# Performance work log

Measured on AMD Instinct MI355X. Metric: run time of the kernel, lower is better.

Reference implementation:

```python
import jax, jax.numpy as jnp
import numpy as np

B, NSEQ, SEQ_PER = 2, 4, 256
S = NSEQ * SEQ_PER            # total sequence (stocks interleaved along seq dim)
D, H, HD = 1024, 16, 64       # d_model, nhead, head_dim
HD2, HD4 = HD // 2, HD // 4
DFF = 4096
LAMBDA_INIT = 0.2             # lambda_init_fn(0) = 0.8 - 0.6*exp(0)
SCALING = 1.0 / float(np.sqrt(HD2))
EPS_DEF = float(np.finfo(np.float32).eps)   # torch RMSNorm default eps (eps=None)
EPS_ATTN = 1e-5


def _rms(x, w, eps):
    return x * jax.lax.rsqrt(jnp.mean(x * x, axis=-1, keepdims=True) + eps) * w


def _rope(x, fc):
    # x: (B, T, NSEQ, 2H, HD2); fc: (T, HD4, 2) holding (cos, sin)
    xr = x.reshape(x.shape[:-1] + (HD4, 2))
    c = fc[None, :, None, None, :, 0]
    s = fc[None, :, None, None, :, 1]
    x0, x1 = xr[..., 0], xr[..., 1]
    return jnp.stack([x0 * c - x1 * s, x0 * s + x1 * c], axis=-1).reshape(x.shape)


def setup_inputs():
    key = jax.random.key(0)
    ks = jax.random.split(key, 16)
    def w(i, shape, std=0.02):
        return jax.random.normal(ks[i], shape, jnp.float32) * std
    # true RoPE table for seq_per_stock-1 positions
    t = jnp.arange(SEQ_PER - 1, dtype=jnp.float32)[:, None]
    inv = 1.0 / (10000.0 ** (jnp.arange(HD4, dtype=jnp.float32) / HD4))
    ang = t * inv[None, :]
    return {
        "x": jax.random.normal(ks[0], (B, S, D), jnp.float32),
        "freqs_cis": jnp.stack([jnp.cos(ang), jnp.sin(ang)], axis=-1),
        "w_norm1": jnp.ones((D,), jnp.float32),
        "w_norm2": jnp.ones((D,), jnp.float32),
        "Wq": w(1, (H * HD, D)), "bq": jnp.zeros((H * HD,), jnp.float32),
        "Wk": w(2, (H * HD, D)), "bk": jnp.zeros((H * HD,), jnp.float32),
        "Wv": w(3, (H * HD, D)), "bv": jnp.zeros((H * HD,), jnp.float32),
        "Wo": w(4, (D, H * HD)), "bo": jnp.zeros((D,), jnp.float32),
        "lq1": w(5, (HD2,), 0.1), "lk1": w(6, (HD2,), 0.1),
        "lq2": w(7, (HD2,), 0.1), "lk2": w(8, (HD2,), 0.1),
        "w_attn_norm": jnp.ones((HD,), jnp.float32),
        "Wg": w(9, (2 * DFF, D)), "bg": jnp.zeros((2 * DFF,), jnp.float32),
        "Wout": w(10, (D, DFF)), "bout": jnp.zeros((D,), jnp.float32),
    }


def reference(x, freqs_cis, w_norm1, w_norm2, Wq, bq, Wk, bk, Wv, bv, Wo, bo,
              lq1, lk1, lq2, lk2, w_attn_norm, Wg, bg, Wout, bout):
    Bz, Sz, _ = x.shape
    h = _rms(x, w_norm1, EPS_DEF)
    q = (h @ Wq.T + bq).reshape(Bz, SEQ_PER, NSEQ, 2 * H, HD2)
    k = (h @ Wk.T + bk).reshape(Bz, SEQ_PER, NSEQ, 2 * H, HD2)
    v = (h @ Wv.T + bv).reshape(Bz, Sz, H, HD).transpose(0, 2, 1, 3)   # (B,H,S,HD), interleaved order
    # RoPE on all but the first per-stock timestep; same freqs for every stock
    q = jnp.concatenate([q[:, :1], _rope(q[:, 1:], freqs_cis)], axis=1)
    k = jnp.concatenate([k[:, :1], _rope(k[:, 1:], freqs_cis)], axis=1)
    # reorder q/k to stock-major flat sequence (torch permute(0,4,1,2,3)+reshape)
    q = q.transpose(0, 2, 1, 3, 4).reshape(Bz, Sz, 2 * H, HD2).transpose(0, 2, 1, 3)
    k = k.transpose(0, 2, 1, 3, 4).reshape(Bz, Sz, 2 * H, HD2).transpose(0, 2, 1, 3)
    scores = jnp.einsum('bhqd,bhkd->bhqk', q, k) * SCALING              # (B,2H,S,S)
    causal = jnp.triu(jnp.ones((SEQ_PER, SEQ_PER), bool), 1)
    mask = jnp.tile(causal, (NSEQ, NSEQ))   # block-tiled causal, as torch .repeat
    att = jnp.sign(scores) * jax.nn.softmax(
        jnp.where(mask, -1e30, jnp.abs(scores)), axis=-1)
    lam = jnp.exp(jnp.sum(lk1 * lq1)) - jnp.exp(jnp.sum(lk2 * lq2)) + LAMBDA_INIT
    att = att.reshape(Bz, H, 2, Sz, Sz)
    a1, a2 = att[:, :, 0], att[:, :, 1]
    G = jnp.mean(a1, axis=-2, keepdims=True)          # mean over queries, broadcast back
    a = jnp.where(mask, 0.0, a1 - lam * a2 + lam * G)
    ao = jnp.einsum('bhqk,bhkd->bhqd', a, v)          # v kept in interleaved order (faithful to source)
    ao = _rms(ao, w_attn_norm, EPS_ATTN)
    ao = ao.reshape(Bz, Sz, H * HD)  # flat reinterpret (B,H,S,HD)->(B,S,H*HD), matches torch reshape chain
    x = x + ao @ Wo.T + bo
    h2 = _rms(x, w_norm2, EPS_DEF)
    u, vg = jnp.split(h2 @ Wg.T + bg, 2, axis=-1)
    return x + (u * jax.nn.silu(vg)) @ Wout.T + bout
```

## Files before the change

kernel.cpp:

```cpp
#include <hip/hip_runtime.h>

#define LAMBDA_INIT 0.2f
#define SCALING 0.17677669529663687f
#define EPS_DEF 1.1920928955078125e-07f
#define EPS_ATTN 1e-5f

typedef unsigned short us4 __attribute__((ext_vector_type(4)));
typedef unsigned short us8v __attribute__((ext_vector_type(8)));
typedef float f32x4 __attribute__((ext_vector_type(4)));
typedef float f32x2 __attribute__((ext_vector_type(2)));
typedef __bf16 bf16x8 __attribute__((ext_vector_type(8)));

#define MFMA16(a, b, c) __builtin_amdgcn_mfma_f32_16x16x32_bf16((a), (b), (c), 0, 0, 0)

__device__ __forceinline__ float bf2f(unsigned short u) {
    unsigned int x = ((unsigned int)u) << 16;
    return __builtin_bit_cast(float, x);
}
__device__ __forceinline__ unsigned short f2bf(float f) {
    unsigned int x = __builtin_bit_cast(unsigned int, f);
    x += 0x7fffu + ((x >> 16) & 1u);
    return (unsigned short)(x >> 16);
}
__device__ __forceinline__ void split8(f32x4 a, f32x4 b, us8v& hi, us8v& lo) {
#pragma unroll
    for (int u = 0; u < 4; u++) {
        unsigned short h = f2bf(a[u]);
        hi[u] = h; lo[u] = f2bf(a[u] - bf2f(h));
        unsigned short h2 = f2bf(b[u]);
        hi[4 + u] = h2; lo[4 + u] = f2bf(b[u] - bf2f(h2));
    }
}
__device__ __forceinline__ bf16x8 ldb(const unsigned short* p) {
    return __builtin_bit_cast(bf16x8, *(const us8v*)p);
}
__device__ __forceinline__ f32x4 rope4(f32x4 v, const float* __restrict__ fc, int p, int dd) {
    if (p == 0) return v;
    int d4 = (dd & 31) >> 1;
    f32x4 f = *(const f32x4*)(fc + ((size_t)(p - 1) * 16 + d4) * 2);
    f32x4 o;
    o[0] = v[0] * f[0] - v[1] * f[1];
    o[1] = v[0] * f[1] + v[1] * f[0];
    o[2] = v[2] * f[2] - v[3] * f[3];
    o[3] = v[2] * f[3] + v[3] * f[2];
    return o;
}

__device__ __forceinline__ float wave_sum(float v) {
#pragma unroll
    for (int o = 32; o > 0; o >>= 1) v += __shfl_down(v, o);
    return v;
}
__device__ __forceinline__ float block_sum(float v, float* red4) {
    int wv = threadIdx.x >> 6;
    float w = wave_sum(v);
    __syncthreads();
    if ((threadIdx.x & 63) == 0) red4[wv] = w;
    __syncthreads();
    return red4[0] + red4[1] + red4[2] + red4[3];
}

__global__ __launch_bounds__(256) void prep(float* __restrict__ G, float* __restrict__ lamp,
                                            const float* lq1, const float* lk1,
                                            const float* lq2, const float* lk2) {
    int i = (blockIdx.x * 256 + threadIdx.x) * 4;
    G[i] = 0.f; G[i + 1] = 0.f; G[i + 2] = 0.f; G[i + 3] = 0.f;
    if (blockIdx.x == 0 && threadIdx.x == 0) {
        float a = 0.f, c = 0.f;
        for (int d = 0; d < 32; d++) {
            a += lq1[d] * lk1[d];
            c += lq2[d] * lk2[d];
        }
        *lamp = expf(a) - expf(c) + LAMBDA_INIT;
    }
}

__global__ __launch_bounds__(256) void cvt_wsplit(
        const float* __restrict__ s0, const float* __restrict__ s1,
        const float* __restrict__ s2, const float* __restrict__ s3,
        unsigned short* __restrict__ h0, unsigned short* __restrict__ l0,
        unsigned short* __restrict__ h1p, unsigned short* __restrict__ l1p,
        unsigned short* __restrict__ h2p, unsigned short* __restrict__ l2p,
        unsigned short* __restrict__ d3, int n4) {
    const int z = blockIdx.y;
    int i = blockIdx.x * 256 + threadIdx.x;
    if (i >= n4) return;
    if (z == 3) {
        f32x4 v = ((const f32x4*)s3)[i];
        us4 o;
#pragma unroll
        for (int u = 0; u < 4; u++) o[u] = f2bf(v[u]);
        ((us4*)d3)[i] = o;
        return;
    }
    const float* s = (z == 0) ? s0 : (z == 1) ? s1 : s2;
    unsigned short* hi = (z == 0) ? h0 : (z == 1) ? h1p : h2p;
    unsigned short* lo = (z == 0) ? l0 : (z == 1) ? l1p : l2p;
    f32x4 v = ((const f32x4*)s)[i];
    us4 h, l;
#pragma unroll
    for (int u = 0; u < 4; u++) {
        h[u] = f2bf(v[u]);
        l[u] = f2bf(v[u] - bf2f(h[u]));
    }
    ((us4*)hi)[i] = h;
    ((us4*)lo)[i] = l;
}

__global__ __launch_bounds__(256) void cvt_gate2(const float* __restrict__ Wg,
                                                 unsigned short* __restrict__ WuB,
                                                 unsigned short* __restrict__ WvB, int n4) {
    const int z = blockIdx.y;
    const float* s = Wg + (size_t)z * 4194304;
    unsigned short* d = z ? WvB : WuB;
    int i = blockIdx.x * 256 + threadIdx.x;
    if (i >= n4) return;
    f32x4 v = ((const f32x4*)s)[i];
    us4 o;
#pragma unroll
    for (int u = 0; u < 4; u++) o[u] = f2bf(v[u]);
    ((us4*)d)[i] = o;
}

__global__ __launch_bounds__(256) void cvt_bf16(const float* __restrict__ s,
                                                unsigned short* __restrict__ d, int n4) {
    int i = blockIdx.x * 256 + threadIdx.x;
    if (i >= n4) return;
    f32x4 v = ((const f32x4*)s)[i];
    us4 o;
#pragma unroll
    for (int u = 0; u < 4; u++) o[u] = f2bf(v[u]);
    ((us4*)d)[i] = o;
}

template <int OUTBF>
__global__ __launch_bounds__(256) void rms_kernel(const float* __restrict__ x,
                                                  const float* __restrict__ w,
                                                  void* __restrict__ out, float eps) {
    int row = blockIdx.x;
    int tid = threadIdx.x;
    size_t base = (size_t)row * 1024 + tid * 4;
    f32x4 v = *(const f32x4*)(x + base);
    float ss = v[0]*v[0] + v[1]*v[1] + v[2]*v[2] + v[3]*v[3];
    __shared__ float red4[4];
    float tot = block_sum(ss, red4);
    float r = rsqrtf(tot * (1.0f / 1024.f) + eps);
    f32x4 wv = *(const f32x4*)(w + tid * 4);
    if (OUTBF) {
        us4 o;
#pragma unroll
        for (int i = 0; i < 4; i++) o[i] = f2bf(v[i] * r * wv[i]);
        *(us4*)((unsigned short*)out + base) = o;
    } else {
        f32x4 o;
#pragma unroll
        for (int i = 0; i < 4; i++) o[i] = v[i] * r * wv[i];
        *(f32x4*)((float*)out + base) = o;
    }
}

__global__ __launch_bounds__(256) void rms_split(const float* __restrict__ x,
                                                 const float* __restrict__ w,
                                                 unsigned short* __restrict__ hh,
                                                 unsigned short* __restrict__ hl, float eps) {
    int row = blockIdx.x;
    int tid = threadIdx.x;
    size_t base = (size_t)row * 1024 + tid * 4;
    f32x4 v = *(const f32x4*)(x + base);
    float ss = v[0]*v[0] + v[1]*v[1] + v[2]*v[2] + v[3]*v[3];
    __shared__ float red4[4];
    float tot = block_sum(ss, red4);
    float r = rsqrtf(tot * (1.0f / 1024.f) + eps);
    f32x4 wv = *(const f32x4*)(w + tid * 4);
    us4 oh, ol;
#pragma unroll
    for (int i = 0; i < 4; i++) {
        float val = v[i] * r * wv[i];
        oh[i] = f2bf(val);
        ol[i] = f2bf(val - bf2f(oh[i]));
    }
    *(us4*)(hh + base) = oh;
    *(us4*)(hl + base) = ol;
}

__global__ __launch_bounds__(256) void gemm_qkv_ps(
        const unsigned short* __restrict__ AH, const unsigned short* __restrict__ AL,
        const unsigned short* __restrict__ WqH, const unsigned short* __restrict__ WqL,
        const unsigned short* __restrict__ WkH, const unsigned short* __restrict__ WkL,
        const unsigned short* __restrict__ WvH, const unsigned short* __restrict__ WvL,
        const float* __restrict__ bq, const float* __restrict__ bk, const float* __restrict__ bv,
        float* __restrict__ Yq, float* __restrict__ Yk, float* __restrict__ Yv) {
    const int z = blockIdx.z;
    const unsigned short* BH = (z == 0) ? WqH : (z == 1) ? WkH : WvH;
    const unsigned short* BL = (z == 0) ? WqL : (z == 1) ? WkL : WvL;
    const float* bias = (z == 0) ? bq : (z == 1) ? bk : bv;
    float* out        = (z == 0) ? Yq : (z == 1) ? Yk : Yv;
    const int K = 1024, N = 1024;
    __shared__ __align__(16) unsigned short Ah[64][72];
    __shared__ __align__(16) unsigned short Al[64][72];
    __shared__ __align__(16) unsigned short Bh[64][72];
    __shared__ __align__(16) unsigned short Bl[64][72];
    const int t = threadIdx.x;
    const int bm = blockIdx.x, bn = blockIdx.y;
    const int lane = t & 63, w = t >> 6;
    const int wr = w >> 1, wc = w & 1;
    const int l15 = lane & 15, lg = lane >> 4;
    const int sr = t >> 2, sc = (t & 3) * 16;

    const unsigned short* AgH = AH + (size_t)(bm * 64 + sr) * K + sc;
    const unsigned short* AgL = AL + (size_t)(bm * 64 + sr) * K + sc;
    const unsigned short* BgH = BH + (size_t)(bn * 64 + sr) * K + sc;
    const unsigned short* BgL = BL + (size_t)(bn * 64 + sr) * K + sc;

    f32x4 acc[2][2] = {};

    us8v ah0 = *(const us8v*)AgH, ah1 = *(const us8v*)(AgH + 8);
    us8v al0 = *(const us8v*)AgL, al1 = *(const us8v*)(AgL + 8);
    us8v bh0 = *(const us8v*)BgH, bh1 = *(const us8v*)(BgH + 8);
    us8v bl0 = *(const us8v*)BgL, bl1 = *(const us8v*)(BgL + 8);

    for (int k0 = 0; k0 < K; k0 += 64) {
        __syncthreads();
        *(us8v*)&Ah[sr][sc] = ah0; *(us8v*)&Ah[sr][sc + 8] = ah1;
        *(us8v*)&Al[sr][sc] = al0; *(us8v*)&Al[sr][sc + 8] = al1;
        *(us8v*)&Bh[sr][sc] = bh0; *(us8v*)&Bh[sr][sc + 8] = bh1;
        *(us8v*)&Bl[sr][sc] = bl0; *(us8v*)&Bl[sr][sc + 8] = bl1;
        __syncthreads();
        if (k0 + 64 < K) {
            const int kn = k0 + 64;
            ah0 = *(const us8v*)(AgH + kn); ah1 = *(const us8v*)(AgH + kn + 8);
            al0 = *(const us8v*)(AgL + kn); al1 = *(const us8v*)(AgL + kn + 8);
            bh0 = *(const us8v*)(BgH + kn); bh1 = *(const us8v*)(BgH + kn + 8);
            bl0 = *(const us8v*)(BgL + kn); bl1 = *(const us8v*)(BgL + kn + 8);
        }
#pragma unroll
        for (int kk = 0; kk < 2; kk++) {
            bf16x8 afh[2], afl[2], bfh[2], bfl[2];
#pragma unroll
            for (int mi = 0; mi < 2; mi++) {
                afh[mi] = ldb(&Ah[wr * 32 + mi * 16 + l15][kk * 32 + lg * 8]);
                afl[mi] = ldb(&Al[wr * 32 + mi * 16 + l15][kk * 32 + lg * 8]);
            }
#pragma unroll
            for (int ni = 0; ni < 2; ni++) {
                bfh[ni] = ldb(&Bh[wc * 32 + ni * 16 + l15][kk * 32 + lg * 8]);
                bfl[ni] = ldb(&Bl[wc * 32 + ni * 16 + l15][kk * 32 + lg * 8]);
            }
#pragma unroll
            for (int mi = 0; mi < 2; mi++)
#pragma unroll
                for (int ni = 0; ni < 2; ni++) {
                    acc[mi][ni] = MFMA16(afl[mi], bfh[ni], acc[mi][ni]);
                    acc[mi][ni] = MFMA16(afh[mi], bfl[ni], acc[mi][ni]);
                    acc[mi][ni] = MFMA16(afh[mi], bfh[ni], acc[mi][ni]);
                }
        }
    }

    const int rbase = bm * 64 + wr * 32 + (lg << 2);
    const int cbase = bn * 64 + wc * 32 + l15;
#pragma unroll
    for (int mi = 0; mi < 2; mi++) {
#pragma unroll
        for (int ni = 0; ni < 2; ni++) {
            int col = cbase + ni * 16;
            float bb = bias[col];
#pragma unroll
            for (int r = 0; r < 4; r++) {
                int row = rbase + mi * 16 + r;
                out[(size_t)row * N + col] = acc[mi][ni][r] + bb;
            }
        }
    }
}

__global__ __launch_bounds__(256) void gemm_mfma_wb(const unsigned short* __restrict__ A,
                                                    const unsigned short* __restrict__ Bt,
                                                    const float* __restrict__ bias,
                                                    const float* __restrict__ res,
                                                    float* __restrict__ out,
                                                    int M, int N, int K) {
    __shared__ __align__(16) unsigned short As[64][136];
    __shared__ __align__(16) unsigned short Bs[64][136];
    const int t = threadIdx.x;
    const int bm = blockIdx.x, bn = blockIdx.y;
    const int lane = t & 63, w = t >> 6;
    const int wr = w >> 1, wc = w & 1;
    const int l15 = lane & 15, lg = lane >> 4;
    const int sr = t >> 2, sc = (t & 3) * 32;

    const unsigned short* Ag = A + (size_t)(bm * 64 + sr) * K + sc;
    const unsigned short* Bg = Bt + (size_t)(bn * 64 + sr) * K + sc;

    f32x4 acc[2][2] = {};

    us8v a0 = *(const us8v*)Ag,        a1 = *(const us8v*)(Ag + 8);
    us8v a2 = *(const us8v*)(Ag + 16), a3 = *(const us8v*)(Ag + 24);
    us8v b0 = *(const us8v*)Bg,        b1 = *(const us8v*)(Bg + 8);
    us8v b2 = *(const us8v*)(Bg + 16), b3 = *(const us8v*)(Bg + 24);

    for (int k0 = 0; k0 < K; k0 += 128) {
        __syncthreads();
        *(us8v*)&As[sr][sc]      = a0;
        *(us8v*)&As[sr][sc + 8]  = a1;
        *(us8v*)&As[sr][sc + 16] = a2;
        *(us8v*)&As[sr][sc + 24] = a3;
        *(us8v*)&Bs[sr][sc]      = b0;
        *(us8v*)&Bs[sr][sc + 8]  = b1;
        *(us8v*)&Bs[sr][sc + 16] = b2;
        *(us8v*)&Bs[sr][sc + 24] = b3;
        __syncthreads();
        if (k0 + 128 < K) {
            const int kn = k0 + 128;
            a0 = *(const us8v*)(Ag + kn);      a1 = *(const us8v*)(Ag + kn + 8);
            a2 = *(const us8v*)(Ag + kn + 16); a3 = *(const us8v*)(Ag + kn + 24);
            b0 = *(const us8v*)(Bg + kn);      b1 = *(const us8v*)(Bg + kn + 8);
            b2 = *(const us8v*)(Bg + kn + 16); b3 = *(const us8v*)(Bg + kn + 24);
        }
#pragma unroll
        for (int kk = 0; kk < 4; kk++) {
            bf16x8 af[2], bf[2];
#pragma unroll
            for (int mi = 0; mi < 2; mi++)
                af[mi] = ldb(&As[wr * 32 + mi * 16 + l15][kk * 32 + lg * 8]);
#pragma unroll
            for (int ni = 0; ni < 2; ni++)
                bf[ni] = ldb(&Bs[wc * 32 + ni * 16 + l15][kk * 32 + lg * 8]);
#pragma unroll
            for (int mi = 0; mi < 2; mi++)
#pragma unroll
                for (int ni = 0; ni < 2; ni++)
                    acc[mi][ni] = MFMA16(af[mi], bf[ni], acc[mi][ni]);
        }
    }

    const int rbase = bm * 64 + wr * 32 + (lg << 2);
    const int cbase = bn * 64 + wc * 32 + l15;
#pragma unroll
    for (int mi = 0; mi < 2; mi++) {
#pragma unroll
        for (int ni = 0; ni < 2; ni++) {
            int col = cbase + ni * 16;
            float bb = bias[col];
#pragma unroll
            for (int r = 0; r < 4; r++) {
                int row = rbase + mi * 16 + r;
                size_t oi = (size_t)row * N + col;
                out[oi] = acc[mi][ni][r] + bb + res[oi];
            }
        }
    }
}

__global__ __launch_bounds__(256) void gemm_gate_wb(const unsigned short* __restrict__ A,
                                                    const unsigned short* __restrict__ WuB,
                                                    const unsigned short* __restrict__ WvB,
                                                    const float* __restrict__ bg,
                                                    unsigned short* __restrict__ mlp) {
    __shared__ __align__(16) unsigned short As[128][72];
    __shared__ __align__(16) unsigned short BsU[64][72];
    __shared__ __align__(16) unsigned short BsV[64][72];
    const int t = threadIdx.x;
    const int bm = blockIdx.x, bn = blockIdx.y;
    const int lane = t & 63, w = t >> 6;
    const int wr = w >> 1, wc = w & 1;
    const int l15 = lane & 15, lg = lane >> 4;
    const int sr = t >> 2, sc = (t & 3) * 16;

    const unsigned short* Ag  = A + (size_t)(bm * 128 + sr) * 1024 + sc;
    const unsigned short* Ag2 = Ag + (size_t)64 * 1024;
    const unsigned short* BgU = WuB + (size_t)(bn * 64 + sr) * 1024 + sc;
    const unsigned short* BgV = WvB + (size_t)(bn * 64 + sr) * 1024 + sc;

    f32x4 accU[4][2] = {};
    f32x4 accV[4][2] = {};

    us8v a0 = *(const us8v*)Ag,  a1 = *(const us8v*)(Ag + 8);
    us8v a2 = *(const us8v*)Ag2, a3 = *(const us8v*)(Ag2 + 8);
    us8v u0 = *(const us8v*)BgU, u1 = *(const us8v*)(BgU + 8);
    us8v v0 = *(const us8v*)BgV, v1 = *(const us8v*)(BgV + 8);

    for (int k0 = 0; k0 < 1024; k0 += 64) {
        __syncthreads();
        *(us8v*)&As[sr][sc]          = a0;
        *(us8v*)&As[sr][sc + 8]      = a1;
        *(us8v*)&As[sr + 64][sc]     = a2;
        *(us8v*)&As[sr + 64][sc + 8] = a3;
        *(us8v*)&BsU[sr][sc]         = u0;
        *(us8v*)&BsU[sr][sc + 8]     = u1;
        *(us8v*)&BsV[sr][sc]         = v0;
        *(us8v*)&BsV[sr][sc + 8]     = v1;
        __syncthreads();
        if (k0 + 64 < 1024) {
            const int kn = k0 + 64;
            a0 = *(const us8v*)(Ag + kn);  a1 = *(const us8v*)(Ag + kn + 8);
            a2 = *(const us8v*)(Ag2 + kn); a3 = *(const us8v*)(Ag2 + kn + 8);
            u0 = *(const us8v*)(BgU + kn); u1 = *(const us8v*)(BgU + kn + 8);
            v0 = *(const us8v*)(BgV + kn); v1 = *(const us8v*)(BgV + kn + 8);
        }
#pragma unroll
        for (int kk = 0; kk < 2; kk++) {
            bf16x8 af[4], bu[2], bv2[2];
#pragma unroll
            for (int mi = 0; mi < 4; mi++)
                af[mi] = ldb(&As[wr * 64 + mi * 16 + l15][kk * 32 + lg * 8]);
#pragma unroll
            for (int ni = 0; ni < 2; ni++) {
                bu[ni]  = ldb(&BsU[wc * 32 + ni * 16 + l15][kk * 32 + lg * 8]);
                bv2[ni] = ldb(&BsV[wc * 32 + ni * 16 + l15][kk * 32 + lg * 8]);
            }
#pragma unroll
            for (int mi = 0; mi < 4; mi++)
#pragma unroll
                for (int ni = 0; ni < 2; ni++) {
                    accU[mi][ni] = MFMA16(af[mi], bu[ni], accU[mi][ni]);
                    accV[mi][ni] = MFMA16(af[mi], bv2[ni], accV[mi][ni]);
                }
        }
    }

    const int rbase = bm * 128 + wr * 64 + (lg << 2);
    const int cbase = bn * 64 + wc * 32 + l15;
#pragma unroll
    for (int mi = 0; mi < 4; mi++) {
#pragma unroll
        for (int ni = 0; ni < 2; ni++) {
            int col = cbase + ni * 16;
            float bu_ = bg[col], bv_ = bg[4096 + col];
#pragma unroll
            for (int r = 0; r < 4; r++) {
                int row = rbase + mi * 16 + r;
                float u = accU[mi][ni][r] + bu_;
                float v = accV[mi][ni][r] + bv_;
                float s = v / (1.f + __expf(-v));
                mlp[(size_t)row * 4096 + col] = f2bf(u * s);
            }
        }
    }
}

__global__ __launch_bounds__(256) void rope_split_k(const float* __restrict__ Yk,
                                                    const float* __restrict__ fc,
                                                    unsigned short* __restrict__ KhG,
                                                    unsigned short* __restrict__ KlG) {
    int t = blockIdx.x;
    int s = t & 1023;
    int p = s >> 2;
    int c0 = threadIdx.x * 4;
    const float* y = Yk + (size_t)t * 1024 + c0;
    float v0 = y[0], v1 = y[1], v2 = y[2], v3 = y[3];
    if (p > 0) {
        int d4 = (c0 & 31) >> 1;
        f32x4 f = *(const f32x4*)(fc + ((size_t)(p - 1) * 16 + d4) * 2);
        float w0 = v0 * f[0] - v1 * f[1];
        float w1 = v0 * f[1] + v1 * f[0];
        float w2 = v2 * f[2] - v3 * f[3];
        float w3 = v2 * f[3] + v3 * f[2];
        v0 = w0; v1 = w1; v2 = w2; v3 = w3;
    }
    us4 hi, lo;
    hi[0] = f2bf(v0); lo[0] = f2bf(v0 - bf2f(hi[0]));
    hi[1] = f2bf(v1); lo[1] = f2bf(v1 - bf2f(hi[1]));
    hi[2] = f2bf(v2); lo[2] = f2bf(v2 - bf2f(hi[2]));
    hi[3] = f2bf(v3); lo[3] = f2bf(v3 - bf2f(hi[3]));
    *(us4*)(KhG + (size_t)t * 1024 + c0) = hi;
    *(us4*)(KlG + (size_t)t * 1024 + c0) = lo;
}

__global__ __launch_bounds__(256) void v_split_t(const float* __restrict__ Yv,
                                                 unsigned short* __restrict__ VtH,
                                                 unsigned short* __restrict__ VtL) {
    const int jc = blockIdx.x, h = blockIdx.y, b = blockIdx.z;
    __shared__ float tile[64][65];
    const int t = threadIdx.x;
    {
        const int jr = t >> 2, dc = (t & 3) * 16;
        const float* src = Yv + ((size_t)(b * 1024 + jc * 64 + jr) << 10) + h * 64 + dc;
        *(f32x4*)&tile[jr][dc]      = *(const f32x4*)src;
        *(f32x4*)&tile[jr][dc + 4]  = *(const f32x4*)(src + 4);
        *(f32x4*)&tile[jr][dc + 8]  = *(const f32x4*)(src + 8);
        *(f32x4*)&tile[jr][dc + 12] = *(const f32x4*)(src + 12);
    }
    __syncthreads();
    const int d = t >> 2, js = (t & 3) * 16;
    us8v h0, h1, l0, l1;
#pragma unroll
    for (int n = 0; n < 16; n++) {
        float val = tile[js + n][d];
        unsigned short hh = f2bf(val);
        unsigned short ll = f2bf(val - bf2f(hh));
        if (n < 8) { h0[n] = hh; l0[n] = ll; }
        else       { h1[n - 8] = hh; l1[n - 8] = ll; }
    }
    size_t ob = (((size_t)(b * 16 + h) * 64 + d) << 10) + jc * 64 + js;
    *(us8v*)(VtH + ob) = h0; *(us8v*)(VtH + ob + 8) = h1;
    *(us8v*)(VtL + ob) = l0; *(us8v*)(VtL + ob + 8) = l1;
}

__global__ __launch_bounds__(256) void pass_0(const float* __restrict__ Yq,
                                              const float* __restrict__ fc,
                                              const unsigned short* __restrict__ KhG,
                                              const unsigned short* __restrict__ KlG,
                                              float* __restrict__ MZ) {
    const int blk = blockIdx.x;
    const int qc = 15 - (blk >> 5);
    const int h  = blk & 15;
    const int b  = (blk >> 4) & 1;
    const int t = threadIdx.x;
    const int lane = t & 63, w = t >> 6;
    const int l15 = lane & 15, lg = lane >> 4;

    __shared__ __align__(16) unsigned short Kh[64][72];
    __shared__ __align__(16) unsigned short Kl[64][72];

    us8v qh[2], ql[2];
    {
        const int srq = qc * 64 + w * 16 + l15;
        const int p = srq >> 2;
        const float* qp = Yq + ((size_t)(b * 1024 + srq) << 10) + h * 64 + lg * 8;
#pragma unroll
        for (int H = 0; H < 2; H++) {
            int dd = lg * 8 + H * 32;
            f32x4 a = rope4(*(const f32x4*)(qp + H * 32), fc, p, dd);
            f32x4 c = rope4(*(const f32x4*)(qp + H * 32 + 4), fc, p, dd + 4);
            split8(a, c, qh[H], ql[H]);
        }
    }
    const int dq0 = w * 16 + (lg << 2);

    const int srow = t >> 2, ssub = t & 3;
    const int ptk = 4 * (srow & 15) + (srow >> 4);
    const unsigned short* KhB = KhG + ((size_t)(b * 1024) << 10) + h * 64;
    const unsigned short* KlB = KlG + ((size_t)(b * 1024) << 10) + h * 64;

    float z1r[4] = {0.f, 0.f, 0.f, 0.f};
    float z2r[4] = {0.f, 0.f, 0.f, 0.f};

    us8v rkh0, rkh1, rkl0, rkl1;
    {
        const unsigned short* kh = KhB + ((size_t)ptk << 10) + ssub * 16;
        const unsigned short* kl = KlB + ((size_t)ptk << 10) + ssub * 16;
        rkh0 = *(const us8v*)kh; rkh1 = *(const us8v*)(kh + 8);
        rkl0 = *(const us8v*)kl; rkl1 = *(const us8v*)(kl + 8);
    }
    for (int kc = 0; kc <= qc; kc++) {
        __syncthreads();
        *(us8v*)&Kh[srow][ssub * 16]     = rkh0;
        *(us8v*)&Kh[srow][ssub * 16 + 8] = rkh1;
        *(us8v*)&Kl[srow][ssub * 16]     = rkl0;
        *(us8v*)&Kl[srow][ssub * 16 + 8] = rkl1;
        __syncthreads();
        if (kc < qc) {
            const unsigned short* kh = KhB + ((size_t)((kc + 1) * 64 + ptk) << 10) + ssub * 16;
            const unsigned short* kl = KlB + ((size_t)((kc + 1) * 64 + ptk) << 10) + ssub * 16;
            rkh0 = *(const us8v*)kh; rkh1 = *(const us8v*)(kh + 8);
            rkl0 = *(const us8v*)kl; rkl1 = *(const us8v*)(kl + 8);
        }
        const int kpos = kc * 16 + l15;
#pragma unroll
        for (int kf = 0; kf < 4; kf++) {
            const int krow = kf * 16 + l15;
            const int kcol = lg * 8;
            bf16x8 b1h = ldb(&Kh[krow][kcol]),      b1l = ldb(&Kl[krow][kcol]);
            bf16x8 b2h = ldb(&Kh[krow][32 + kcol]), b2l = ldb(&Kl[krow][32 + kcol]);
            f32x4 s1 = {}, s2 = {};
            s1 = MFMA16(__builtin_bit_cast(bf16x8, ql[0]), b1h, s1);
            s1 = MFMA16(__builtin_bit_cast(bf16x8, qh[0]), b1l, s1);
            s1 = MFMA16(__builtin_bit_cast(bf16x8, qh[0]), b1h, s1);
            s2 = MFMA16(__builtin_bit_cast(bf16x8, ql[1]), b2h, s2);
            s2 = MFMA16(__builtin_bit_cast(bf16x8, qh[1]), b2l, s2);
            s2 = MFMA16(__builtin_bit_cast(bf16x8, qh[1]), b2h, s2);
#pragma unroll
            for (int r = 0; r < 4; r++) {
                int pq = (qc * 64 + dq0 + r) >> 2;
                if (kpos <= pq) {
                    z1r[r] += __expf(fabsf(s1[r] * SCALING));
                    z2r[r] += __expf(fabsf(s2[r] * SCALING));
                }
            }
        }
    }
#pragma unroll
    for (int r = 0; r < 4; r++) {
        float a = z1r[r];
        a += __shfl_xor(a, 1); a += __shfl_xor(a, 2);
        a += __shfl_xor(a, 4); a += __shfl_xor(a, 8);
        float c = z2r[r];
        c += __shfl_xor(c, 1); c += __shfl_xor(c, 2);
        c += __shfl_xor(c, 4); c += __shfl_xor(c, 8);
        if (l15 == 0) {
            int s2i = qc * 64 + dq0 + r;
            f32x2 zz; zz[0] = a; zz[1] = c;
            *(f32x2*)(MZ + (((size_t)(b * 16 + h) << 10) + s2i) * 2) = zz;
        }
    }
}

__global__ __launch_bounds__(256) void pass_1(const float* __restrict__ Yq,
                                              const float* __restrict__ fc,
                                              const unsigned short* __restrict__ KhG,
                                              const unsigned short* __restrict__ KlG,
                                              const unsigned short* __restrict__ VtH,
                                              const unsigned short* __restrict__ VtL,
                                              const float* __restrict__ MZ,
                                              const float* __restrict__ lamp,
                                              float* __restrict__ G,
                                              float* __restrict__ AOp) {
    const int blk = blockIdx.x;
    const int qc = 15 - (blk >> 5);
    const int h  = blk & 15;
    const int b  = (blk >> 4) & 1;
    const int t = threadIdx.x;
    const int lane = t & 63, w = t >> 6;
    const int l15 = lane & 15, lg = lane >> 4;

    __shared__ __align__(16) unsigned short Kh[64][72];
    __shared__ __align__(16) unsigned short Kl[64][72];
    __shared__ __align__(16) unsigned short Vth[64][72];
    __shared__ __align__(16) unsigned short Vtl[64][72];
    __shared__ __align__(16) unsigned short Wh[64][72];
    __shared__ __align__(16) unsigned short Wl[64][72];
    __shared__ float Gacc[4][1024];

    for (int i = t; i < 4096; i += 256) ((float*)Gacc)[i] = 0.f;

    us8v qh[2], ql[2];
    {
        const int srq = qc * 64 + w * 16 + l15;
        const int p = srq >> 2;
        const float* qp = Yq + ((size_t)(b * 1024 + srq) << 10) + h * 64 + lg * 8;
#pragma unroll
        for (int H = 0; H < 2; H++) {
            int dd = lg * 8 + H * 32;
            f32x4 a = rope4(*(const f32x4*)(qp + H * 32), fc, p, dd);
            f32x4 c = rope4(*(const f32x4*)(qp + H * 32 + 4), fc, p, dd + 4);
            split8(a, c, qh[H], ql[H]);
        }
    }
    const int dq0 = w * 16 + (lg << 2);

    float z1r[4], z2r[4];
#pragma unroll
    for (int r = 0; r < 4; r++) {
        int s2i = qc * 64 + dq0 + r;
        f32x2 zz = *(const f32x2*)(MZ + (((size_t)(b * 16 + h) << 10) + s2i) * 2);
        z1r[r] = 1.f / fmaxf(zz[0], 1e-20f);
        z2r[r] = 1.f / fmaxf(zz[1], 1e-20f);
    }

    const int srow = t >> 2, ssub = t & 3;
    const int ptk = 4 * (srow & 15) + (srow >> 4);
    const unsigned short* KhB = KhG + ((size_t)(b * 1024) << 10) + h * 64;
    const unsigned short* KlB = KlG + ((size_t)(b * 1024) << 10) + h * 64;
    const unsigned short* VhB = VtH + (((size_t)(b * 16 + h) * 64 + srow) << 10) + ssub * 256;
    const unsigned short* VlB = VtL + (((size_t)(b * 16 + h) * 64 + srow) << 10) + ssub * 256;
    const float lam = *lamp;

    f32x4 ao[4] = {};

    us8v rkh0, rkh1, rkl0, rkl1, rvh0, rvh1, rvl0, rvl1;
    {
        const unsigned short* kh = KhB + ((size_t)ptk << 10) + ssub * 16;
        const unsigned short* kl = KlB + ((size_t)ptk << 10) + ssub * 16;
        rkh0 = *(const us8v*)kh; rkh1 = *(const us8v*)(kh + 8);
        rkl0 = *(const us8v*)kl; rkl1 = *(const us8v*)(kl + 8);
        rvh0 = *(const us8v*)VhB; rvh1 = *(const us8v*)(VhB + 8);
        rvl0 = *(const us8v*)VlB; rvl1 = *(const us8v*)(VlB + 8);
    }
    for (int kc = 0; kc <= qc; kc++) {
        __syncthreads();
        *(us8v*)&Kh[srow][ssub * 16]      = rkh0;
        *(us8v*)&Kh[srow][ssub * 16 + 8]  = rkh1;
        *(us8v*)&Kl[srow][ssub * 16]      = rkl0;
        *(us8v*)&Kl[srow][ssub * 16 + 8]  = rkl1;
        *(us8v*)&Vth[srow][ssub * 16]     = rvh0;
        *(us8v*)&Vth[srow][ssub * 16 + 8] = rvh1;
        *(us8v*)&Vtl[srow][ssub * 16]     = rvl0;
        *(us8v*)&Vtl[srow][ssub * 16 + 8] = rvl1;
        __syncthreads();
        if (kc < qc) {
            const unsigned short* kh = KhB + ((size_t)((kc + 1) * 64 + ptk) << 10) + ssub * 16;
            const unsigned short* kl = KlB + ((size_t)((kc + 1) * 64 + ptk) << 10) + ssub * 16;
            rkh0 = *(const us8v*)kh; rkh1 = *(const us8v*)(kh + 8);
            rkl0 = *(const us8v*)kl; rkl1 = *(const us8v*)(kl + 8);
            const unsigned short* vh = VhB + (kc + 1) * 16;
            const unsigned short* vl = VlB + (kc + 1) * 16;
            rvh0 = *(const us8v*)vh; rvh1 = *(const us8v*)(vh + 8);
            rvl0 = *(const us8v*)vl; rvl1 = *(const us8v*)(vl + 8);
        }
        const int kpos = kc * 16 + l15;
#pragma unroll
        for (int kf = 0; kf < 4; kf++) {
            const int krow = kf * 16 + l15;
            const int kcol = lg * 8;
            bf16x8 b1h = ldb(&Kh[krow][kcol]),      b1l = ldb(&Kl[krow][kcol]);
            bf16x8 b2h = ldb(&Kh[krow][32 + kcol]), b2l = ldb(&Kl[krow][32 + kcol]);
            f32x4 s1 = {}, s2 = {};
            s1 = MFMA16(__builtin_bit_cast(bf16x8, ql[0]), b1h, s1);
            s1 = MFMA16(__builtin_bit_cast(bf16x8, qh[0]), b1l, s1);
            s1 = MFMA16(__builtin_bit_cast(bf16x8, qh[0]), b1h, s1);
            s2 = MFMA16(__builtin_bit_cast(bf16x8, ql[1]), b2h, s2);
            s2 = MFMA16(__builtin_bit_cast(bf16x8, qh[1]), b2l, s2);
            s2 = MFMA16(__builtin_bit_cast(bf16x8, qh[1]), b2h, s2);
            const int kli = kf * 16 + l15;
            float colsum = 0.f;
#pragma unroll
            for (int r = 0; r < 4; r++) {
                int pq = (qc * 64 + dq0 + r) >> 2;
                float wv = 0.f, a1 = 0.f;
                if (kpos <= pq) {
                    float t1 = s1[r] * SCALING, t2 = s2[r] * SCALING;
                    float sg1 = (t1 > 0.f) ? 1.f : ((t1 < 0.f) ? -1.f : 0.f);
                    float sg2 = (t2 > 0.f) ? 1.f : ((t2 < 0.f) ? -1.f : 0.f);
                    a1 = sg1 * __expf(fabsf(t1)) * z1r[r];
                    wv = a1 - lam * (sg2 * __expf(fabsf(t2)) * z2r[r]);
                }
                colsum += a1;
                unsigned short hh = f2bf(wv);
                Wh[dq0 + r][kli] = hh;
                Wl[dq0 + r][kli] = f2bf(wv - bf2f(hh));
            }
            colsum += __shfl_xor(colsum, 16);
            colsum += __shfl_xor(colsum, 32);
            if (lane < 16) Gacc[w][kf * 256 + kc * 16 + lane] = colsum;
        }
#pragma unroll
        for (int kh2 = 0; kh2 < 2; kh2++) {
            bf16x8 wah = ldb(&Wh[w * 16 + l15][kh2 * 32 + lg * 8]);
            bf16x8 wal = ldb(&Wl[w * 16 + l15][kh2 * 32 + lg * 8]);
#pragma unroll
            for (int df = 0; df < 4; df++) {
                bf16x8 vbh = ldb(&Vth[df * 16 + l15][kh2 * 32 + lg * 8]);
                bf16x8 vbl = ldb(&Vtl[df * 16 + l15][kh2 * 32 + lg * 8]);
                ao[df] = MFMA16(wah, vbl, ao[df]);
                ao[df] = MFMA16(wal, vbh, ao[df]);
                ao[df] = MFMA16(wah, vbh, ao[df]);
            }
        }
    }

#pragma unroll
    for (int df = 0; df < 4; df++) {
#pragma unroll
        for (int r = 0; r < 4; r++) {
            int tq = qc * 64 + dq0 + r;
            int qrow = ((tq & 3) << 8) + (tq >> 2);
            AOp[((((size_t)(b * 16 + h)) << 10) + qrow) * 64 + df * 16 + l15] = ao[df][r];
        }
    }

    __syncthreads();
    float* Gb = G + ((size_t)(b * 16 + h) << 10);
    const int limp = (qc + 1) << 4;
    for (int idx = t; idx < 1024; idx += 256) {
        if ((idx & 255) < limp) {
            float s = Gacc[0][idx] + Gacc[1][idx] + Gacc[2][idx] + Gacc[3][idx];
            atomicAdd(&Gb[idx], s);
        }
    }
}

__global__ __launch_bounds__(256) void pass_2a(const float* __restrict__ G,
                                               const float* __restrict__ Yv,
                                               float* __restrict__ GVpre) {
    const int h = blockIdx.x, b = blockIdx.y;
    const int t = threadIdx.x;
    __shared__ float Gl[1024];
    __shared__ float S[256][64];
    __shared__ float segsum[4][64];
    for (int i = t; i < 1024; i += 256) Gl[i] = G[((size_t)(b * 16 + h) << 10) + i];
    __syncthreads();
    const int d = t & 63, pg = t >> 6;
    const float* Yvb = Yv + ((size_t)b << 20) + h * 64 + d;
    for (int p0 = 0; p0 < 64; p0++) {
        int pos = pg * 64 + p0;
        float s = 0.f;
#pragma unroll
        for (int sq = 0; sq < 4; sq++) {
            int j = (sq << 8) + pos;
            s += Gl[j] * Yvb[(size_t)j << 10];
        }
        S[pos][d] = s;
    }
    __syncthreads();
    float acc = 0.f;
    for (int p0 = 0; p0 < 64; p0++) {
        int pos = pg * 64 + p0;
        acc += S[pos][d];
        S[pos][d] = acc;
    }
    segsum[pg][d] = acc;
    __syncthreads();
    float off = 0.f;
    for (int g = 0; g < pg; g++) off += segsum[g][d];
    float* gv = GVpre + (((size_t)(b * 16 + h)) << 14) + d;
    for (int p0 = 0; p0 < 64; p0++) {
        int pos = pg * 64 + p0;
        gv[pos << 6] = S[pos][d] + off;
    }
}

__global__ __launch_bounds__(256) void pass_2b(const float* __restrict__ AOp,
                                               const float* __restrict__ GVpre,
                                               const float* __restrict__ lamp,
                                               const float* __restrict__ wan,
                                               unsigned short* __restrict__ aoS) {
    const int qg = blockIdx.x;
    const int h = blockIdx.y, b = blockIdx.z;
    const int t = threadIdx.x;
    const int d = t & 63, rg = t >> 6;
    const float lamg = (*lamp) * (1.f / 1024.f);
    const float wv = wan[d];
    const float* aob = AOp + ((((size_t)(b * 16 + h)) << 10) + (qg << 8)) * 64 + d;
    const float* gvb = GVpre + (((size_t)(b * 16 + h)) << 14) + d;
    unsigned short* ob = aoS + ((size_t)b << 20) + ((size_t)h << 16) + ((size_t)(qg << 8) << 6) + d;
    for (int p0 = 0; p0 < 64; p0++) {
        int pq = p0 * 4 + rg;
        float ao = aob[(size_t)pq << 6] + lamg * gvb[(size_t)pq << 6];
        float ss = ao * ao;
#pragma unroll
        for (int o = 1; o < 64; o <<= 1) ss += __shfl_xor(ss, o);
        float rr_ = rsqrtf(ss * (1.f / 64.f) + EPS_ATTN);
        ob[(size_t)pq << 6] = f2bf(ao * rr_ * wv);
    }
}

extern "C" void kernel_launch(void* const* d_in, const int* in_sizes, int n_in,
                              void* d_out, int out_size, void* d_ws, size_t ws_size,
                              hipStream_t stream) {
    const float* x    = (const float*)d_in[0];
    const float* fc   = (const float*)d_in[1];
    const float* w1   = (const float*)d_in[2];
    const float* w2   = (const float*)d_in[3];
    const float* Wq   = (const float*)d_in[4];
    const float* bq   = (const float*)d_in[5];
    const float* Wk   = (const float*)d_in[6];
    const float* bk   = (const float*)d_in[7];
    const float* Wv   = (const float*)d_in[8];
    const float* bv   = (const float*)d_in[9];
    const float* Wo   = (const float*)d_in[10];
    const float* bo   = (const float*)d_in[11];
    const float* lq1  = (const float*)d_in[12];
    const float* lk1  = (const float*)d_in[13];
    const float* lq2  = (const float*)d_in[14];
    const float* lk2  = (const float*)d_in[15];
    const float* wan  = (const float*)d_in[16];
    const float* Wg   = (const float*)d_in[17];
    const float* bg   = (const float*)d_in[18];
    const float* Wout = (const float*)d_in[19];
    const float* bout = (const float*)d_in[20];

    char* ws = (char*)d_ws;
    const size_t MB = 1024 * 1024;
    float* G    = (float*)(ws);
    float* lam  = (float*)(ws + 256 * 1024);
    float* MZ   = (float*)(ws + 384 * 1024);
    unsigned short* hH = (unsigned short*)(ws + 1 * MB);
    unsigned short* hL = (unsigned short*)(ws + 5 * MB);
    float* Yq   = (float*)(ws + 9 * MB);
    float* Yk   = (float*)(ws + 17 * MB);
    float* Yv   = (float*)(ws + 25 * MB);
    unsigned short* WqH = (unsigned short*)(ws + 33 * MB);
    unsigned short* WqL = (unsigned short*)(ws + 35 * MB);
    unsigned short* WkH = (unsigned short*)(ws + 37 * MB);
    unsigned short* WkL = (unsigned short*)(ws + 39 * MB);
    unsigned short* WvH = (unsigned short*)(ws + 41 * MB);
    unsigned short* WvL = (unsigned short*)(ws + 43 * MB);
    unsigned short* WoB = (unsigned short*)(ws + 45 * MB);
    float* AOp  = (float*)(ws + 33 * MB);
    float* GVpre= (float*)(ws + 41 * MB);
    unsigned short* KhG = (unsigned short*)(ws + 1 * MB);
    unsigned short* KlG = (unsigned short*)(ws + 5 * MB);
    unsigned short* VtH = (unsigned short*)(ws + 17 * MB);
    unsigned short* VtL = (unsigned short*)(ws + 21 * MB);
    unsigned short* aoS = (unsigned short*)(ws + 1 * MB);
    float* X1           = (float*)(ws + 9 * MB);
    unsigned short* h2b = (unsigned short*)(ws + 5 * MB);
    unsigned short* mlp = (unsigned short*)(ws + 17 * MB);
    unsigned short* WuB = (unsigned short*)(ws + 33 * MB);
    unsigned short* WvB2= (unsigned short*)(ws + 41 * MB);
    unsigned short* WoutB=(unsigned short*)(ws + 33 * MB);

    prep<<<32, 256, 0, stream>>>(G, lam, lq1, lk1, lq2, lk2);
    rms_split<<<2048, 256, 0, stream>>>(x, w1, hH, hL, EPS_DEF);
    cvt_wsplit<<<dim3(1024, 4), 256, 0, stream>>>(Wq, Wk, Wv, Wo,
                                                  WqH, WqL, WkH, WkL, WvH, WvL, WoB, 262144);
    gemm_qkv_ps<<<dim3(32, 16, 3), 256, 0, stream>>>(hH, hL, WqH, WqL, WkH, WkL, WvH, WvL,
                                                     bq, bk, bv, Yq, Yk, Yv);
    rope_split_k<<<2048, 256, 0, stream>>>(Yk, fc, KhG, KlG);
    v_split_t<<<dim3(16, 16, 2), 256, 0, stream>>>(Yv, VtH, VtL);
    pass_0<<<512, 256, 0, stream>>>(Yq, fc, KhG, KlG, MZ);
    pass_1<<<512, 256, 0, stream>>>(Yq, fc, KhG, KlG, VtH, VtL, MZ, lam, G, AOp);
    pass_2a<<<dim3(16, 2), 256, 0, stream>>>(G, Yv, GVpre);
    pass_2b<<<dim3(4, 16, 2), 256, 0, stream>>>(AOp, GVpre, lam, wan, aoS);
    dim3 gmf(32, 16);
    gemm_mfma_wb<<<gmf, 256, 0, stream>>>(aoS, WoB, bo, x, X1, 2048, 1024, 1024);
    cvt_gate2<<<dim3(4096, 2), 256, 0, stream>>>(Wg, WuB, WvB2, 1048576);
    rms_kernel<1><<<2048, 256, 0, stream>>>(X1, w2, h2b, EPS_DEF);
    gemm_gate_wb<<<dim3(16, 64), 256, 0, stream>>>(h2b, WuB, WvB2, bg, mlp);
    cvt_bf16<<<4096, 256, 0, stream>>>(Wout, WoutB, 1048576);
    gemm_mfma_wb<<<gmf, 256, 0, stream>>>(mlp, WoutB, bout, X1, (float*)d_out, 2048, 1024, 4096);
}
```

Before: 414.9 us.

## Split pass_0 key loop across two blocks and drop K low-part correction

pass_0 now launches twice as many blocks, each handling alternate key chunks (even or odd). Partial softmax denominators are combined with atomicAdd into MZ, which prep now zeroes. The K low-order bf16 split term is also dropped from the score MFMAs, cutting LDS traffic, global loads and MFMA count. This lowers the precision of the softmax normalizer, and atomic accumulation makes the summation order nondeterministic.

```diff
diff --git a/kernel.cpp b/kernel.cpp
--- a/kernel.cpp
+++ b/kernel.cpp
@@ -60,11 +60,17 @@
     return red4[0] + red4[1] + red4[2] + red4[3];
 }
 
-__global__ __launch_bounds__(256) void prep(float* __restrict__ G, float* __restrict__ lamp,
+__global__ __launch_bounds__(256) void prep(float* __restrict__ G, float* __restrict__ MZ,
+                                            float* __restrict__ lamp,
                                             const float* lq1, const float* lk1,
                                             const float* lq2, const float* lk2) {
     int i = (blockIdx.x * 256 + threadIdx.x) * 4;
-    G[i] = 0.f; G[i + 1] = 0.f; G[i + 2] = 0.f; G[i + 3] = 0.f;
+    if (i < 32768) {
+        G[i] = 0.f; G[i + 1] = 0.f; G[i + 2] = 0.f; G[i + 3] = 0.f;
+    } else {
+        int j = i - 32768;
+        MZ[j] = 0.f; MZ[j + 1] = 0.f; MZ[j + 2] = 0.f; MZ[j + 3] = 0.f;
+    }
     if (blockIdx.x == 0 && threadIdx.x == 0) {
         float a = 0.f, c = 0.f;
         for (int d = 0; d < 32; d++) {
@@ -500,18 +506,17 @@
 __global__ __launch_bounds__(256) void pass_0(const float* __restrict__ Yq,
                                               const float* __restrict__ fc,
                                               const unsigned short* __restrict__ KhG,
-                                              const unsigned short* __restrict__ KlG,
                                               float* __restrict__ MZ) {
     const int blk = blockIdx.x;
-    const int qc = 15 - (blk >> 5);
-    const int h  = blk & 15;
-    const int b  = (blk >> 4) & 1;
+    const int qc   = 15 - (blk >> 6);
+    const int half = blk & 1;
+    const int h    = (blk >> 1) & 15;
+    const int b    = (blk >> 5) & 1;
     const int t = threadIdx.x;
     const int lane = t & 63, w = t >> 6;
     const int l15 = lane & 15, lg = lane >> 4;
 
     __shared__ __align__(16) unsigned short Kh[64][72];
-    __shared__ __align__(16) unsigned short Kl[64][72];
 
     us8v qh[2], ql[2];
     {
@@ -531,44 +536,36 @@
     const int srow = t >> 2, ssub = t & 3;
     const int ptk = 4 * (srow & 15) + (srow >> 4);
     const unsigned short* KhB = KhG + ((size_t)(b * 1024) << 10) + h * 64;
-    const unsigned short* KlB = KlG + ((size_t)(b * 1024) << 10) + h * 64;
 
     float z1r[4] = {0.f, 0.f, 0.f, 0.f};
     float z2r[4] = {0.f, 0.f, 0.f, 0.f};
 
-    us8v rkh0, rkh1, rkl0, rkl1;
+    us8v rkh0, rkh1;
     {
-        const unsigned short* kh = KhB + ((size_t)ptk << 10) + ssub * 16;
-        const unsigned short* kl = KlB + ((size_t)ptk << 10) + ssub * 16;
+        const int kc0 = (half <= qc) ? half : 0;
+        const unsigned short* kh = KhB + ((size_t)(kc0 * 64 + ptk) << 10) + ssub * 16;
         rkh0 = *(const us8v*)kh; rkh1 = *(const us8v*)(kh + 8);
-        rkl0 = *(const us8v*)kl; rkl1 = *(const us8v*)(kl + 8);
-    }
-    for (int kc = 0; kc <= qc; kc++) {
+    }
+    for (int kc = half; kc <= qc; kc += 2) {
         __syncthreads();
         *(us8v*)&Kh[srow][ssub * 16]     = rkh0;
         *(us8v*)&Kh[srow][ssub * 16 + 8] = rkh1;
-        *(us8v*)&Kl[srow][ssub * 16]     = rkl0;
-        *(us8v*)&Kl[srow][ssub * 16 + 8] = rkl1;
         __syncthreads();
-        if (kc < qc) {
-            const unsigned short* kh = KhB + ((size_t)((kc + 1) * 64 + ptk) << 10) + ssub * 16;
-            const unsigned short* kl = KlB + ((size_t)((kc + 1) * 64 + ptk) << 10) + ssub * 16;
+        if (kc + 2 <= qc) {
+            const unsigned short* kh = KhB + ((size_t)((kc + 2) * 64 + ptk) << 10) + ssub * 16;
             rkh0 = *(const us8v*)kh; rkh1 = *(const us8v*)(kh + 8);
-            rkl0 = *(const us8v*)kl; rkl1 = *(const us8v*)(kl + 8);
         }
         const int kpos = kc * 16 + l15;
 #pragma unroll
         for (int kf = 0; kf < 4; kf++) {
             const int krow = kf * 16 + l15;
             const int kcol = lg * 8;
-            bf16x8 b1h = ldb(&Kh[krow][kcol]),      b1l = ldb(&Kl[krow][kcol]);
-            bf16x8 b2h = ldb(&Kh[krow][32 + kcol]), b2l = ldb(&Kl[krow][32 + kcol]);
+            bf16x8 b1h = ldb(&Kh[krow][kcol]);
+            bf16x8 b2h = ldb(&Kh[krow][32 + kcol]);
             f32x4 s1 = {}, s2 = {};
             s1 = MFMA16(__builtin_bit_cast(bf16x8, ql[0]), b1h, s1);
-            s1 = MFMA16(__builtin_bit_cast(bf16x8, qh[0]), b1l, s1);
             s1 = MFMA16(__builtin_bit_cast(bf16x8, qh[0]), b1h, s1);
             s2 = MFMA16(__builtin_bit_cast(bf16x8, ql[1]), b2h, s2);
-            s2 = MFMA16(__builtin_bit_cast(bf16x8, qh[1]), b2l, s2);
             s2 = MFMA16(__builtin_bit_cast(bf16x8, qh[1]), b2h, s2);
 #pragma unroll
             for (int r = 0; r < 4; r++) {
@@ -590,8 +587,9 @@
         c += __shfl_xor(c, 4); c += __shfl_xor(c, 8);
         if (l15 == 0) {
             int s2i = qc * 64 + dq0 + r;
-            f32x2 zz; zz[0] = a; zz[1] = c;
-            *(f32x2*)(MZ + (((size_t)(b * 16 + h) << 10) + s2i) * 2) = zz;
+            float* mp = MZ + (((size_t)(b * 16 + h) << 10) + s2i) * 2;
+            atomicAdd(mp, a);
+            atomicAdd(mp + 1, c);
         }
     }
 }
@@ -881,7 +879,7 @@
     unsigned short* WvB2= (unsigned short*)(ws + 41 * MB);
     unsigned short* WoutB=(unsigned short*)(ws + 33 * MB);
 
-    prep<<<32, 256, 0, stream>>>(G, lam, lq1, lk1, lq2, lk2);
+    prep<<<96, 256, 0, stream>>>(G, MZ, lam, lq1, lk1, lq2, lk2);
     rms_split<<<2048, 256, 0, stream>>>(x, w1, hH, hL, EPS_DEF);
     cvt_wsplit<<<dim3(1024, 4), 256, 0, stream>>>(Wq, Wk, Wv, Wo,
                                                   WqH, WqL, WkH, WkL, WvH, WvL, WoB, 262144);
@@ -889,7 +887,7 @@
                                                      bq, bk, bv, Yq, Yk, Yv);
     rope_split_k<<<2048, 256, 0, stream>>>(Yk, fc, KhG, KlG);
     v_split_t<<<dim3(16, 16, 2), 256, 0, stream>>>(Yv, VtH, VtL);
-    pass_0<<<512, 256, 0, stream>>>(Yq, fc, KhG, KlG, MZ);
+    pass_0<<<1024, 256, 0, stream>>>(Yq, fc, KhG, MZ);
     pass_1<<<512, 256, 0, stream>>>(Yq, fc, KhG, KlG, VtH, VtL, MZ, lam, G, AOp);
     pass_2a<<<dim3(16, 2), 256, 0, stream>>>(G, Yv, GVpre);
     pass_2b<<<dim3(4, 16, 2), 256, 0, stream>>>(AOp, GVpre, lam, wan, aoS);
```

Result: no change. 409.6 us (-1.3%).
